# Performance work log

Hardware: AMD Instinct MI355X
Metric: run time of the kernel (lower is better)

The kernel has to match this reference:

```python
import jax, jax.numpy as jnp
import numpy as np

N = 16_777_216        # num_samples
T_MAX = 100_000       # number of distinct event times -> ~168 ties per time


def setup_inputs() -> dict:
    key = jax.random.key(0)
    k1, k2, k3 = jax.random.split(key, 3)
    risk = jax.random.normal(k1, (N,), dtype=jnp.float32)
    event_indicator = jax.random.randint(k2, (N,), 0, 2).astype(jnp.float32)
    # Cox partial likelihood assumes samples sorted by event time (ascending),
    # matching the original module's consecutive tie-grouping while-loop.
    time = jnp.sort(jax.random.randint(k3, (N,), 0, T_MAX, dtype=jnp.int32))
    return {"risk": risk, "event_indicator": event_indicator, "time": time}


def reference(risk, event_indicator, time):
    # Original loop places each tie-group's sum(exp(risk)) at the group's first
    # index (zeros elsewhere) and cumsums.  Equivalently, for each i:
    #   risk_cumsum[i] = sum_{j : time[j] <= time[i]} exp(risk[j])
    # which (time sorted ascending) is the full cumsum of exp(risk) gathered at
    # the LAST index of i's tie group.
    n = risk.shape[0]
    c = jnp.cumsum(jnp.exp(risk))                              # (N,)
    end_idx = jnp.searchsorted(time, time, side="right") - 1    # last idx of each tie group
    risk_cumsum = c[end_idx]                                    # (N,)
    risk_minus = risk - jnp.log(risk_cumsum)
    loss = -(risk_minus * event_indicator).sum() / n
    return loss
```

## Files before the change

kernel.cpp:

```cpp
#include <hip/hip_runtime.h>
#include <math.h>


#define TMAXV   100000
#define NPAD    100352
#define NBLK_SC 98
#define VPT     16
#define NBLK1   2048
#define SENT    0x7fffffff

__device__ __forceinline__ void atomAddF(float* p, float v) {
    unsafeAtomicAdd(p, v);
}

__device__ __forceinline__ float block_reduce_sum(float v, float* lds) {
    const int lane = threadIdx.x & 63;
    const int wid  = threadIdx.x >> 6;
    #pragma unroll
    for (int d = 32; d > 0; d >>= 1) v += __shfl_down(v, d);
    __syncthreads();
    if (lane == 0) lds[wid] = v;
    __syncthreads();
    float r = 0.f;
    if (wid == 0) {
        const int nw = (int)(blockDim.x >> 6);
        r = (lane < nw) ? lds[lane] : 0.f;
        #pragma unroll
        for (int d = 8; d > 0; d >>= 1) r += __shfl_down(r, d);
    }
    return r;
}

__global__ __launch_bounds__(256)
void k1_bucket(const float* __restrict__ risk, const float* __restrict__ ev,
               const int* __restrict__ tim,
               float* __restrict__ S, float* __restrict__ E,
               float* __restrict__ Apart, int n, int per_block) {
    __shared__ float lds[16];
    const int lane  = threadIdx.x & 63;
    const int start = (int)blockIdx.x * per_block;
    int end = start + per_block;
    if (end > n) end = n;
    const int step = (int)blockDim.x * VPT;

    float accA = 0.f;
    for (int i0 = start; i0 < end; i0 += step) {
        const int base = i0 + (int)threadIdx.x * VPT;
        float r[VPT], w[VPT];
        int   t[VPT];
        if (base + VPT <= end) {
            #pragma unroll
            for (int q = 0; q < VPT / 4; ++q) {
                const float4 rr = *(const float4*)(risk + base + 4 * q);
                const float4 ww = *(const float4*)(ev   + base + 4 * q);
                const int4   tt = *(const int4*)(tim   + base + 4 * q);
                r[4*q+0]=rr.x; r[4*q+1]=rr.y; r[4*q+2]=rr.z; r[4*q+3]=rr.w;
                w[4*q+0]=ww.x; w[4*q+1]=ww.y; w[4*q+2]=ww.z; w[4*q+3]=ww.w;
                t[4*q+0]=tt.x; t[4*q+1]=tt.y; t[4*q+2]=tt.z; t[4*q+3]=tt.w;
            }
        } else {
            #pragma unroll
            for (int j = 0; j < VPT; ++j) {
                const int i = base + j;
                const bool ok = (i < end);
                r[j] = ok ? risk[i] : 0.f;
                w[j] = ok ? ev[i]   : 0.f;
                t[j] = ok ? tim[i]  : SENT;
            }
        }

        float ve[VPT];
        #pragma unroll
        for (int j = 0; j < VPT; ++j) {
            ve[j] = __expf(r[j]);
            accA += w[j] * r[j];
        }

        const int head_t = t[0];
        const int tail_t = t[VPT - 1];
        float tsv = 0.f, tsw = 0.f;
        #pragma unroll
        for (int j = 0; j < VPT; ++j) {
            if (t[j] == tail_t) { tsv += ve[j]; tsw += w[j]; }
        }

        float Sv = tsv, Sw = tsw;
        #pragma unroll
        for (int d = 1; d < 64; d <<= 1) {
            const float ov = __shfl_up(Sv, d);
            const float ow = __shfl_up(Sw, d);
            const int   ok = __shfl_up(tail_t, d);
            if (lane >= d && ok == tail_t) { Sv += ov; Sw += ow; }
        }

        float cv = 0.f, cw = 0.f;
        {
            const float pv = __shfl_up(Sv, 1);
            const float pw = __shfl_up(Sw, 1);
            const int   pk = __shfl_up(tail_t, 1);
            if (lane > 0 && pk == head_t) { cv = pv; cw = pw; }
        }

        int   cur_t = head_t;
        float cur_v = cv, cur_w = cw;
        #pragma unroll
        for (int j = 0; j < VPT; ++j) {
            if (t[j] != cur_t) {
                if (cur_t != SENT) {
                    atomAddF(&S[cur_t], cur_v);
                    atomAddF(&E[cur_t], cur_w);
                }
                cur_t = t[j]; cur_v = 0.f; cur_w = 0.f;
            }
            cur_v += ve[j]; cur_w += w[j];
        }
        const int nh = __shfl_down(head_t, 1);
        if ((lane == 63 || nh != tail_t) && cur_t != SENT) {
            atomAddF(&S[cur_t], cur_v);
            atomAddF(&E[cur_t], cur_w);
        }
    }

    const float tot = block_reduce_sum(accA, lds);
    if (threadIdx.x == 0) Apart[blockIdx.x] = tot;
}

__global__ __launch_bounds__(256)
void k2_partials(const float* __restrict__ S, float* __restrict__ partials) {
    __shared__ float lds[16];
    const int base = (int)blockIdx.x * 1024;
    float v = 0.f;
    for (int j = (int)threadIdx.x; j < 1024; j += 256) v += S[base + j];
    const float tot = block_reduce_sum(v, lds);
    if (threadIdx.x == 0) partials[blockIdx.x] = tot;
}

__global__ __launch_bounds__(1024)
void k3_scan_dot(const float* __restrict__ S, const float* __restrict__ E,
                 const float* __restrict__ partials, float* __restrict__ Bacc) {
    __shared__ float lds[16];
    __shared__ float wsum[16];
    __shared__ float s_off;
    const int tid  = (int)threadIdx.x;
    const int lane = tid & 63;
    const int wid  = tid >> 6;
    const int base = (int)blockIdx.x * 1024;

    float p = (tid < (int)blockIdx.x) ? partials[tid] : 0.f;
    const float off = block_reduce_sum(p, lds);
    if (tid == 0) s_off = off;
    __syncthreads();
    const float offset = s_off;

    const float x = S[base + tid];
    float s = x;
    #pragma unroll
    for (int d = 1; d < 64; d <<= 1) {
        const float o = __shfl_up(s, d);
        if (lane >= d) s += o;
    }
    if (lane == 63) wsum[wid] = s;
    __syncthreads();
    if (wid == 0) {
        float ws = (lane < 16) ? wsum[lane] : 0.f;
        #pragma unroll
        for (int d = 1; d < 16; d <<= 1) {
            const float o = __shfl_up(ws, d);
            if (lane >= d) ws += o;
        }
        if (lane < 16) wsum[lane] = ws;
    }
    __syncthreads();
    const float incl = s + (wid > 0 ? wsum[wid - 1] : 0.f);
    const float P = offset + incl;

    const float w = E[base + tid];
    const float c = (w != 0.f) ? w * __logf(P) : 0.f;
    const float tot = block_reduce_sum(c, lds);
    if (tid == 0) atomAddF(Bacc, tot);
}

__global__ __launch_bounds__(256)
void k4_final(const float* __restrict__ Apart, const float* __restrict__ B,
              float* __restrict__ out, float inv_n) {
    __shared__ float lds[16];
    float v = 0.f;
    for (int j = (int)threadIdx.x; j < NBLK1; j += 256) v += Apart[j];
    const float tot = block_reduce_sum(v, lds);
    if (threadIdx.x == 0) out[0] = -(tot - B[0]) * inv_n;
}

extern "C" void kernel_launch(void* const* d_in, const int* in_sizes, int n_in,
                              void* d_out, int out_size, void* d_ws, size_t ws_size,
                              hipStream_t stream) {
    const float* risk = (const float*)d_in[0];
    const float* ev   = (const float*)d_in[1];
    const int*   tim  = (const int*)d_in[2];
    float* out = (float*)d_out;
    const int n = in_sizes[0];

    float* S        = (float*)d_ws;
    float* E        = S + NPAD;
    float* partials = E + NPAD;
    float* Apart    = partials + 128;
    float* B        = Apart + NBLK1;

    hipMemsetAsync(d_ws, 0, (size_t)(2 * NPAD + 128 + NBLK1 + 2) * sizeof(float), stream);

    const int threads = 256;
    const int win = threads * VPT;
    int per_block = (n + NBLK1 - 1) / NBLK1;
    per_block = ((per_block + win - 1) / win) * win;

    hipLaunchKernelGGL(k1_bucket, dim3(NBLK1), dim3(threads), 0, stream,
                       risk, ev, tim, S, E, Apart, n, per_block);
    hipLaunchKernelGGL(k2_partials, dim3(NBLK_SC), dim3(256), 0, stream, S, partials);
    hipLaunchKernelGGL(k3_scan_dot, dim3(NBLK_SC), dim3(1024), 0, stream, S, E, partials, B);
    hipLaunchKernelGGL(k4_final, dim3(1), dim3(256), 0, stream, Apart, B, out, 1.0f / (float)n);
}
```

Measured before the change: 55.15 us.

## Replace per-group atomics with plain stores and a boundary fixup pass

Each wavefront now stores tie groups that lie strictly inside its span straight into S/E, since no other wavefront can touch them. Only the first and last group of each wavefront, which may span neighbours, go to side buffers. A new small kernel adds those side entries into S/E with atomics. The grid becomes fixed two-window blocks instead of a per-block loop. This removes almost all global float atomics at the cost of an extra launch and extra workspace. It also assumes every interior group is covered by one wavefront and that the side buffers are fully written for every slot.

```diff
diff --git a/kernel.cpp b/kernel.cpp
--- a/kernel.cpp
+++ b/kernel.cpp
@@ -6,7 +6,9 @@
 #define NPAD    100352
 #define NBLK_SC 98
 #define VPT     16
+#define NWIN    2
 #define NBLK1   2048
+#define NS      (NBLK1 * NWIN * 4)
 #define SENT    0x7fffffff
 
 __device__ __forceinline__ void atomAddF(float* p, float v) {
@@ -35,20 +37,27 @@
 void k1_bucket(const float* __restrict__ risk, const float* __restrict__ ev,
                const int* __restrict__ tim,
                float* __restrict__ S, float* __restrict__ E,
-               float* __restrict__ Apart, int n, int per_block) {
-    __shared__ float lds[16];
-    const int lane  = threadIdx.x & 63;
-    const int start = (int)blockIdx.x * per_block;
-    int end = start + per_block;
-    if (end > n) end = n;
-    const int step = (int)blockDim.x * VPT;
+               float* __restrict__ Apart,
+               int* __restrict__ tF, float* __restrict__ vF, float* __restrict__ wF,
+               int* __restrict__ tL, float* __restrict__ vL, float* __restrict__ wL,
+               int n) {
+    __shared__ float lds[16];
+    const int tid   = (int)threadIdx.x;
+    const int lane  = tid & 63;
+    const int start = (int)blockIdx.x * (NWIN * 256 * VPT);
+    int end_blk = start + NWIN * 256 * VPT;
+    if (end_blk > n) end_blk = n;
 
     float accA = 0.f;
-    for (int i0 = start; i0 < end; i0 += step) {
-        const int base = i0 + (int)threadIdx.x * VPT;
+
+    #pragma unroll
+    for (int win = 0; win < NWIN; ++win) {
+        const int base = start + win * (256 * VPT) + tid * VPT;
+        const int sid  = (((int)blockIdx.x * NWIN + win) << 2) | (tid >> 6);
+
         float r[VPT], w[VPT];
         int   t[VPT];
-        if (base + VPT <= end) {
+        if (base + VPT <= end_blk) {
             #pragma unroll
             for (int q = 0; q < VPT / 4; ++q) {
                 const float4 rr = *(const float4*)(risk + base + 4 * q);
@@ -62,7 +71,7 @@
             #pragma unroll
             for (int j = 0; j < VPT; ++j) {
                 const int i = base + j;
-                const bool ok = (i < end);
+                const bool ok = (i < end_blk);
                 r[j] = ok ? risk[i] : 0.f;
                 w[j] = ok ? ev[i]   : 0.f;
                 t[j] = ok ? tim[i]  : SENT;
@@ -78,6 +87,9 @@
 
         const int head_t = t[0];
         const int tail_t = t[VPT - 1];
+        const int sfirst = __shfl(head_t, 0);
+        const int slast  = __shfl(tail_t, 63);
+
         float tsv = 0.f, tsw = 0.f;
         #pragma unroll
         for (int j = 0; j < VPT; ++j) {
@@ -101,28 +113,53 @@
             if (lane > 0 && pk == head_t) { cv = pv; cw = pw; }
         }
 
+        auto route = [&](int tt, float sv, float sw) {
+            if (tt == SENT) return;
+            if (tt == sfirst)      { tF[sid] = tt; vF[sid] = sv; wF[sid] = sw; }
+            else if (tt == slast)  { tL[sid] = tt; vL[sid] = sv; wL[sid] = sw; }
+            else                   { S[tt] = sv;   E[tt] = sw; }
+        };
+
         int   cur_t = head_t;
         float cur_v = cv, cur_w = cw;
         #pragma unroll
         for (int j = 0; j < VPT; ++j) {
             if (t[j] != cur_t) {
-                if (cur_t != SENT) {
-                    atomAddF(&S[cur_t], cur_v);
-                    atomAddF(&E[cur_t], cur_w);
-                }
+                route(cur_t, cur_v, cur_w);
                 cur_t = t[j]; cur_v = 0.f; cur_w = 0.f;
             }
             cur_v += ve[j]; cur_w += w[j];
         }
+
         const int nh = __shfl_down(head_t, 1);
-        if ((lane == 63 || nh != tail_t) && cur_t != SENT) {
-            atomAddF(&S[cur_t], cur_v);
-            atomAddF(&E[cur_t], cur_w);
+        if (lane < 63) {
+            if (nh != tail_t) route(cur_t, cur_v, cur_w);
+        } else {
+            if (sfirst == slast) {
+                tF[sid] = cur_t; vF[sid] = cur_v; wF[sid] = cur_w;
+                tL[sid] = SENT;
+            } else {
+                tL[sid] = cur_t; vL[sid] = cur_v; wL[sid] = cur_w;
+            }
         }
     }
 
     const float tot = block_reduce_sum(accA, lds);
-    if (threadIdx.x == 0) Apart[blockIdx.x] = tot;
+    if (tid == 0) Apart[blockIdx.x] = tot;
+}
+
+__global__ __launch_bounds__(256)
+void k1b_fix(const int* __restrict__ tF, const float* __restrict__ vF,
+             const float* __restrict__ wF,
+             const int* __restrict__ tL, const float* __restrict__ vL,
+             const float* __restrict__ wL,
+             float* __restrict__ S, float* __restrict__ E) {
+    const int i = (int)blockIdx.x * 256 + (int)threadIdx.x;
+    if (i >= NS) return;
+    const int a = tF[i];
+    if (a != SENT) { atomAddF(&S[a], vF[i]); atomAddF(&E[a], wF[i]); }
+    const int b = tL[i];
+    if (b != SENT) { atomAddF(&S[b], vL[i]); atomAddF(&E[b], wL[i]); }
 }
 
 __global__ __launch_bounds__(256)
@@ -204,16 +241,22 @@
     float* partials = E + NPAD;
     float* Apart    = partials + 128;
     float* B        = Apart + NBLK1;
+    int*   tF       = (int*)(B + 2);
+    float* vF       = (float*)(tF + NS);
+    float* wF       = vF + NS;
+    int*   tL       = (int*)(wF + NS);
+    float* vL       = (float*)(tL + NS);
+    float* wL       = vL + NS;
 
     hipMemsetAsync(d_ws, 0, (size_t)(2 * NPAD + 128 + NBLK1 + 2) * sizeof(float), stream);
 
-    const int threads = 256;
-    const int win = threads * VPT;
-    int per_block = (n + NBLK1 - 1) / NBLK1;
-    per_block = ((per_block + win - 1) / win) * win;
-
-    hipLaunchKernelGGL(k1_bucket, dim3(NBLK1), dim3(threads), 0, stream,
-                       risk, ev, tim, S, E, Apart, n, per_block);
+    const int elems_per_block = NWIN * 256 * VPT;
+    const int blocks = (n + elems_per_block - 1) / elems_per_block;
+
+    hipLaunchKernelGGL(k1_bucket, dim3(blocks), dim3(256), 0, stream,
+                       risk, ev, tim, S, E, Apart, tF, vF, wF, tL, vL, wL, n);
+    hipLaunchKernelGGL(k1b_fix, dim3((NS + 255) / 256), dim3(256), 0, stream,
+                       tF, vF, wF, tL, vL, wL, S, E);
     hipLaunchKernelGGL(k2_partials, dim3(NBLK_SC), dim3(256), 0, stream, S, partials);
     hipLaunchKernelGGL(k3_scan_dot, dim3(NBLK_SC), dim3(1024), 0, stream, S, E, partials, B);
     hipLaunchKernelGGL(k4_final, dim3(1), dim3(256), 0, stream, Apart, B, out, 1.0f / (float)n);
```

New measurement: 74.16 us. +34.5%, slower.

## Restructure bucket kernel loads for per-wave contiguous coalesced float4 access

Applied to the files above, without the earlier changes.

Reorganizes the first kernel so each wave processes a contiguous 1024-element chunk as four 256-element sub-segments, with each lane loading 4 contiguous elements per sub-segment. This makes each vector load instruction cover a contiguous span across the wave instead of lane-strided 16-element blocks. In exchange the segmented wave scan over tie keys runs four times per iteration and run boundaries per thread become more frequent, adding shuffle work and some extra atomics.

```diff
diff --git a/kernel.cpp b/kernel.cpp
--- a/kernel.cpp
+++ b/kernel.cpp
@@ -2,10 +2,8 @@
 #include <math.h>
 
 
-#define TMAXV   100000
 #define NPAD    100352
 #define NBLK_SC 98
-#define VPT     16
 #define NBLK1   2048
 #define SENT    0x7fffffff
 
@@ -37,87 +35,94 @@
                float* __restrict__ S, float* __restrict__ E,
                float* __restrict__ Apart, int n, int per_block) {
     __shared__ float lds[16];
-    const int lane  = threadIdx.x & 63;
+    const int lane = (int)threadIdx.x & 63;
+    const int wid  = (int)threadIdx.x >> 6;
     const int start = (int)blockIdx.x * per_block;
     int end = start + per_block;
     if (end > n) end = n;
-    const int step = (int)blockDim.x * VPT;
 
     float accA = 0.f;
-    for (int i0 = start; i0 < end; i0 += step) {
-        const int base = i0 + (int)threadIdx.x * VPT;
-        float r[VPT], w[VPT];
-        int   t[VPT];
-        if (base + VPT <= end) {
-            #pragma unroll
-            for (int q = 0; q < VPT / 4; ++q) {
-                const float4 rr = *(const float4*)(risk + base + 4 * q);
-                const float4 ww = *(const float4*)(ev   + base + 4 * q);
-                const int4   tt = *(const int4*)(tim   + base + 4 * q);
-                r[4*q+0]=rr.x; r[4*q+1]=rr.y; r[4*q+2]=rr.z; r[4*q+3]=rr.w;
-                w[4*q+0]=ww.x; w[4*q+1]=ww.y; w[4*q+2]=ww.z; w[4*q+3]=ww.w;
-                t[4*q+0]=tt.x; t[4*q+1]=tt.y; t[4*q+2]=tt.z; t[4*q+3]=tt.w;
-            }
-        } else {
-            #pragma unroll
-            for (int j = 0; j < VPT; ++j) {
-                const int i = base + j;
-                const bool ok = (i < end);
-                r[j] = ok ? risk[i] : 0.f;
-                w[j] = ok ? ev[i]   : 0.f;
-                t[j] = ok ? tim[i]  : SENT;
+
+    for (int i0 = start; i0 < end; i0 += 4096) {
+        const int sbase = i0 + wid * 1024;
+
+        float r[4][4], w[4][4];
+        int   t[4][4];
+        #pragma unroll
+        for (int q = 0; q < 4; ++q) {
+            const int base = sbase + q * 256 + lane * 4;
+            if (base + 4 <= end) {
+                const float4 rr = *(const float4*)(risk + base);
+                const float4 ww = *(const float4*)(ev   + base);
+                const int4   tt = *(const int4*)(tim   + base);
+                r[q][0]=rr.x; r[q][1]=rr.y; r[q][2]=rr.z; r[q][3]=rr.w;
+                w[q][0]=ww.x; w[q][1]=ww.y; w[q][2]=ww.z; w[q][3]=ww.w;
+                t[q][0]=tt.x; t[q][1]=tt.y; t[q][2]=tt.z; t[q][3]=tt.w;
+            } else {
+                #pragma unroll
+                for (int j = 0; j < 4; ++j) {
+                    const int i = base + j;
+                    const bool ok = (i < end);
+                    r[q][j] = ok ? risk[i] : 0.f;
+                    w[q][j] = ok ? ev[i]   : 0.f;
+                    t[q][j] = ok ? tim[i]  : SENT;
+                }
             }
         }
 
-        float ve[VPT];
-        #pragma unroll
-        for (int j = 0; j < VPT; ++j) {
-            ve[j] = __expf(r[j]);
-            accA += w[j] * r[j];
-        }
-
-        const int head_t = t[0];
-        const int tail_t = t[VPT - 1];
-        float tsv = 0.f, tsw = 0.f;
-        #pragma unroll
-        for (int j = 0; j < VPT; ++j) {
-            if (t[j] == tail_t) { tsv += ve[j]; tsw += w[j]; }
-        }
-
-        float Sv = tsv, Sw = tsw;
-        #pragma unroll
-        for (int d = 1; d < 64; d <<= 1) {
-            const float ov = __shfl_up(Sv, d);
-            const float ow = __shfl_up(Sw, d);
-            const int   ok = __shfl_up(tail_t, d);
-            if (lane >= d && ok == tail_t) { Sv += ov; Sw += ow; }
-        }
-
-        float cv = 0.f, cw = 0.f;
-        {
-            const float pv = __shfl_up(Sv, 1);
-            const float pw = __shfl_up(Sw, 1);
-            const int   pk = __shfl_up(tail_t, 1);
-            if (lane > 0 && pk == head_t) { cv = pv; cw = pw; }
-        }
-
-        int   cur_t = head_t;
-        float cur_v = cv, cur_w = cw;
-        #pragma unroll
-        for (int j = 0; j < VPT; ++j) {
-            if (t[j] != cur_t) {
-                if (cur_t != SENT) {
-                    atomAddF(&S[cur_t], cur_v);
-                    atomAddF(&E[cur_t], cur_w);
+        #pragma unroll
+        for (int q = 0; q < 4; ++q) {
+            float ve[4];
+            #pragma unroll
+            for (int j = 0; j < 4; ++j) {
+                ve[j] = __expf(r[q][j]);
+                accA += w[q][j] * r[q][j];
+            }
+
+            const int head_t = t[q][0];
+            const int tail_t = t[q][3];
+
+            float tsv = 0.f, tsw = 0.f;
+            #pragma unroll
+            for (int j = 0; j < 4; ++j) {
+                if (t[q][j] == tail_t) { tsv += ve[j]; tsw += w[q][j]; }
+            }
+
+            float Sv = tsv, Sw = tsw;
+            #pragma unroll
+            for (int d = 1; d < 64; d <<= 1) {
+                const float ov = __shfl_up(Sv, d);
+                const float ow = __shfl_up(Sw, d);
+                const int   ok = __shfl_up(tail_t, d);
+                if (lane >= d && ok == tail_t) { Sv += ov; Sw += ow; }
+            }
+
+            float cv = 0.f, cw = 0.f;
+            {
+                const float pv = __shfl_up(Sv, 1);
+                const float pw = __shfl_up(Sw, 1);
+                const int   pk = __shfl_up(tail_t, 1);
+                if (lane > 0 && pk == head_t) { cv = pv; cw = pw; }
+            }
+
+            int   cur_t = head_t;
+            float cur_v = cv, cur_w = cw;
+            #pragma unroll
+            for (int j = 0; j < 4; ++j) {
+                if (t[q][j] != cur_t) {
+                    if (cur_t != SENT) {
+                        atomAddF(&S[cur_t], cur_v);
+                        atomAddF(&E[cur_t], cur_w);
+                    }
+                    cur_t = t[q][j]; cur_v = 0.f; cur_w = 0.f;
                 }
-                cur_t = t[j]; cur_v = 0.f; cur_w = 0.f;
-            }
-            cur_v += ve[j]; cur_w += w[j];
-        }
-        const int nh = __shfl_down(head_t, 1);
-        if ((lane == 63 || nh != tail_t) && cur_t != SENT) {
-            atomAddF(&S[cur_t], cur_v);
-            atomAddF(&E[cur_t], cur_w);
+                cur_v += ve[j]; cur_w += w[q][j];
+            }
+            const int nh = __shfl_down(head_t, 1);
+            if ((lane == 63 || nh != tail_t) && cur_t != SENT) {
+                atomAddF(&S[cur_t], cur_v);
+                atomAddF(&E[cur_t], cur_w);
+            }
         }
     }
 
@@ -207,12 +212,11 @@
 
     hipMemsetAsync(d_ws, 0, (size_t)(2 * NPAD + 128 + NBLK1 + 2) * sizeof(float), stream);
 
-    const int threads = 256;
-    const int win = threads * VPT;
+    const int win = 4096;
     int per_block = (n + NBLK1 - 1) / NBLK1;
     per_block = ((per_block + win - 1) / win) * win;
 
-    hipLaunchKernelGGL(k1_bucket, dim3(NBLK1), dim3(threads), 0, stream,
+    hipLaunchKernelGGL(k1_bucket, dim3(NBLK1), dim3(256), 0, stream,
                        risk, ev, tim, S, E, Apart, n, per_block);
     hipLaunchKernelGGL(k2_partials, dim3(NBLK_SC), dim3(256), 0, stream, S, partials);
     hipLaunchKernelGGL(k3_scan_dot, dim3(NBLK_SC), dim3(1024), 0, stream, S, E, partials, B);
```

New measurement: 60.76 us. 1.1x slower.
